# Performance work log

Hardware: AMD Instinct MI355X
Metric: run time of the kernel (lower is better)

Reference implementation:

```python
import math
import jax
import jax.numpy as jnp
import numpy as np

LMAX = 6                 # lmax
F8, F2 = 16, 64          # f_out//8, f_out//2 for f_out=128
DIM6 = sum((2 * l + 1) ** 2 for l in range(LMAX + 1))  # 455 = dim of so3_irreps(6)
NA = NB = NG = 16        # SO(3) activation grid (alpha, beta, gamma)
B, T, H, C = 32, 16, 4, 128


def _real_sh(lmax, xyz):
    # real spherical harmonics: (N,3) unit vectors -> (N,(lmax+1)^2), m=-l..l per l
    x, y, z = xyz[:, 0], xyz[:, 1], xyz[:, 2]
    st = np.sqrt(np.clip(1.0 - z * z, 0.0, None))
    phi = np.arctan2(y, x)
    n = xyz.shape[0]
    P = np.zeros((lmax + 1, lmax + 1, n))
    P[0, 0] = 1.0
    for m in range(1, lmax + 1):
        P[m, m] = -(2 * m - 1) * st * P[m - 1, m - 1]
    for m in range(lmax):
        P[m + 1, m] = (2 * m + 1) * z * P[m, m]
    for m in range(lmax + 1):
        for l in range(m + 2, lmax + 1):
            P[l, m] = ((2 * l - 1) * z * P[l - 1, m] - (l + m - 1) * P[l - 2, m]) / (l - m)
    cols = []
    for l in range(lmax + 1):
        for m in range(-l, l + 1):
            am = abs(m)
            K = math.sqrt((2 * l + 1) / (4 * math.pi) * math.factorial(l - am) / math.factorial(l + am))
            if m > 0:
                cols.append(math.sqrt(2.0) * K * np.cos(m * phi) * P[l, m])
            elif m < 0:
                cols.append(math.sqrt(2.0) * K * np.sin(am * phi) * P[l, am])
            else:
                cols.append(K * P[l, 0])
    return np.stack(cols, axis=-1)


def _flat_wigner(lmax, Rs):
    # component-normalized flat real Wigner-D basis: (G,3,3) -> (G, sum_l (2l+1)^2)
    # D_l(R) solved from Y_l(R x) = D_l(R) Y_l(x) by least squares in float64
    rng = np.random.default_rng(0)
    pts = rng.normal(size=(32, 3))
    pts /= np.linalg.norm(pts, axis=1, keepdims=True)
    Y = _real_sh(lmax, pts)                                     # (32,(lmax+1)^2)
    rp = np.einsum('gij,nj->gni', Rs, pts).reshape(-1, 3)
    Yr = _real_sh(lmax, rp).reshape(len(Rs), 32, -1)            # (G,32,(lmax+1)^2)
    blocks = []
    for l in range(lmax + 1):
        d = 2 * l + 1
        o = l * l
        Apinv = np.linalg.pinv(Y[:, o:o + d])                   # (d,32)
        D = np.einsum('kn,gnm->gmk', Apinv, Yr[:, :, o:o + d])  # (G,d,d)
        blocks.append(math.sqrt(d) * D.reshape(len(Rs), d * d))
    return np.concatenate(blocks, axis=-1)


def _rz(a):
    c, s = np.cos(a), np.sin(a)
    z, o = np.zeros_like(a), np.ones_like(a)
    return np.stack([np.stack([c, -s, z], -1), np.stack([s, c, z], -1), np.stack([z, z, o], -1)], -2)


def _ry(a):
    c, s = np.cos(a), np.sin(a)
    z, o = np.zeros_like(a), np.ones_like(a)
    return np.stack([np.stack([c, z, s], -1), np.stack([z, o, z], -1), np.stack([-s, z, c], -1)], -2)


def _so3_grid():
    # ZYZ Euler grid, Gauss-Legendre in beta; rotations (G,3,3) + Haar weights (G,) summing to 1
    nodes, wts = np.polynomial.legendre.leggauss(NB)
    betas = np.arccos(nodes)
    alphas = np.arange(NA) * 2 * np.pi / NA
    gammas = np.arange(NG) * 2 * np.pi / NG
    Aa, Bb, Cg = np.meshgrid(alphas, betas, gammas, indexing='ij')
    Rs = _rz(Aa.ravel()) @ _ry(Bb.ravel()) @ _rz(Cg.ravel())
    w = np.broadcast_to(wts[None, :, None], (NA, NB, NG)).ravel().copy()
    w *= (2 * np.pi / NA) * (2 * np.pi / NG) / (8 * np.pi ** 2)
    return Rs, w


def _ico_rotations():
    # the 60 rotations of the icosahedral group, generated by closure
    phi = (1.0 + 5.0 ** 0.5) / 2.0
    def rot(axis, ang):
        a = np.asarray(axis, dtype=np.float64)
        a = a / np.linalg.norm(a)
        K = np.array([[0.0, -a[2], a[1]], [a[2], 0.0, -a[0]], [-a[1], a[0], 0.0]])
        return np.eye(3) + math.sin(ang) * K + (1.0 - math.cos(ang)) * (K @ K)
    gens = [rot([0.0, 1.0, phi], 2.0 * np.pi / 5.0), rot([0.0, 0.0, 1.0], np.pi)]
    elems = [np.eye(3)]
    seen = {tuple(np.round(np.eye(3), 5).ravel())}
    frontier = list(elems)
    while frontier:
        nxt = []
        for R in frontier:
            for g in gens:
                Q = g @ R
                k = tuple(np.round(Q, 5).ravel())
                if k not in seen:
                    seen.add(k)
                    elems.append(Q)
                    nxt.append(Q)
        frontier = nxt
    return np.stack(elems)


def _equi_linear(xl, wl):
    # e3nn-style per-irrep linear: xl (...,f_in,u,m), wl (f_in,f_out,u,v); fan_in = f_in*u
    fan_in = wl.shape[0] * wl.shape[2]
    return jnp.einsum('...fum,fguv->...gvm', xl, wl) / np.sqrt(fan_in)


def _forward(x, trajectory, w1s, w1v, w2, D_in, D_outw, ico_wigners):
    b, t, _ = trajectory.shape
    # pack '1x0e+3x1e': scalar = traj[...,9], vectors = traj[...,:9]
    s = trajectory[..., 9][..., None, None, None]       # (b,t,f=1,u=1,m=1)
    v = trajectory[..., :9].reshape(b, t, 1, 3, 3)      # (b,t,f=1,u=3,m=3)
    h = jnp.concatenate([_equi_linear(s, w1s).reshape(b, t, F8, 1),
                         _equi_linear(v, w1v).reshape(b, t, F8, 9)], axis=-1)  # (b,t,16,10)
    # SO(3) activation: coeffs -> grid signal -> relu -> coeffs (lmax 1 -> 6)
    sig = jax.nn.relu(jnp.einsum('btci,gi->btcg', h, D_in))
    h = jnp.einsum('btcg,gi->btci', sig, D_outw)        # (b,t,16,455)
    # per-l equivariant linear, f 16 -> 64
    outs = []
    o = 0
    for l in range(LMAX + 1):
        d = 2 * l + 1
        xl = h[..., o:o + d * d].reshape(b, t, F8, d, d)
        outs.append(_equi_linear(xl, w2[l]).reshape(b, t, F2, d * d))
        o += d * d
    traj = jnp.concatenate(outs, axis=-1)               # (b,t,64,455)
    traj = jnp.einsum('bhcj,ij->bhci', traj, ico_wigners)  # sample on ico rotations
    xg = jnp.einsum('bhcj,ij->bhci', x, ico_wigners)
    return xg, traj


def setup_inputs():
    key = jax.random.key(0)
    ks = jax.random.split(key, 11)
    Rs, w = _so3_grid()
    D_in = _flat_wigner(1, Rs).astype(np.float32)                      # (G,10)
    D_outw = (_flat_wigner(LMAX, Rs) * w[:, None]).astype(np.float32)  # (G,455)
    ico = _flat_wigner(LMAX, _ico_rotations()).astype(np.float32)      # (60,455)
    inp = dict(
        x=jax.random.normal(ks[0], (B, H, C, DIM6), jnp.float32),
        trajectory=jax.random.normal(ks[1], (B, T, 10), jnp.float32),
        w1s=jax.random.normal(ks[2], (1, F8, 1, 1), jnp.float32),
        w1v=jax.random.normal(ks[3], (1, F8, 3, 3), jnp.float32),
        D_in=jnp.asarray(D_in),
        D_outw=jnp.asarray(D_outw),
        ico_wigners=jnp.asarray(ico),
    )
    for l in range(LMAX + 1):
        inp['w2_%d' % l] = jax.random.normal(ks[4 + l], (F8, F2, 2 * l + 1, 2 * l + 1), jnp.float32)
    return inp


def reference(x, trajectory, w1s, w1v, w2_0, w2_1, w2_2, w2_3, w2_4, w2_5, w2_6, D_in, D_outw, ico_wigners):
    w2 = [w2_0, w2_1, w2_2, w2_3, w2_4, w2_5, w2_6]
    return _forward(x, trajectory, w1s, w1v, w2, D_in, D_outw, ico_wigners)
```

## Files before the change

kernel.cpp:

```cpp
#include <hip/hip_runtime.h>
#include <math.h>


#define NBT  512
#define F8c  16
#define F2c  64
#define GJ   455
#define GG   4096
#define NICO 60
#define JP   512

typedef short bf16x8 __attribute__((ext_vector_type(8)));
typedef float f32x4  __attribute__((ext_vector_type(4)));
typedef unsigned int u32;
typedef unsigned short ushort;

struct W7 { const float* p[7]; };

__device__ __forceinline__ ushort f2bf(float f) {
  u32 u = __float_as_uint(f);
  return (ushort)((u + 0x7fffu + ((u >> 16) & 1u)) >> 16);
}

__device__ __forceinline__ int sel7(int l, int a0, int a1, int a2, int a3,
                                    int a4, int a5, int a6) {
  int r = a6;
  r = (l == 5) ? a5 : r; r = (l == 4) ? a4 : r; r = (l == 3) ? a3 : r;
  r = (l == 2) ? a2 : r; r = (l == 1) ? a1 : r; r = (l == 0) ? a0 : r;
  return r;
}
__device__ __forceinline__ float sel7f(int l, float a0, float a1, float a2,
                                       float a3, float a4, float a5, float a6) {
  float r = a6;
  r = (l == 5) ? a5 : r; r = (l == 4) ? a4 : r; r = (l == 3) ? a3 : r;
  r = (l == 2) ? a2 : r; r = (l == 1) ? a1 : r; r = (l == 0) ? a0 : r;
  return r;
}

__global__ __launch_bounds__(256) void k_pre(const float* __restrict__ traj,
                                             const float* __restrict__ w1s,
                                             const float* __restrict__ w1v,
                                             const float* __restrict__ ico,
                                             const float* __restrict__ Dout,
                                             W7 w2,
                                             float* __restrict__ h,
                                             ushort* __restrict__ icoB,
                                             ushort* __restrict__ icoBx,
                                             ushort* __restrict__ DoutBT,
                                             ushort* __restrict__ Abuf,
                                             ushort* __restrict__ Bbuf) {
  __shared__ float t[64][65];
  int b = blockIdx.x, tid = threadIdx.x;
  if (b < 2240) {
    ((uint4*)Abuf)[b * 256 + tid] = (uint4){0, 0, 0, 0};
  } else if (b < 2752) {
    int b2 = b - 2240;
    int jt = b2 & 7, kt = b2 >> 3;
    int tx = tid & 63, ty = tid >> 6;
    #pragma unroll
    for (int i = 0; i < 16; ++i) {
      int r = i * 4 + ty, j = jt * 64 + tx;
      t[r][tx] = (j < GJ) ? Dout[(size_t)(kt * 64 + r) * GJ + j] : 0.f;
    }
    __syncthreads();
    #pragma unroll
    for (int i = 0; i < 16; ++i) {
      int jl = i * 4 + ty;
      DoutBT[(size_t)(jt * 64 + jl) * GG + kt * 64 + tx] = f2bf(t[tx][jl]);
    }
  } else if (b < 4992) {
    int ee = (b - 2752) * 256 + tid;
    if (ee < 573440) {
      int l = (ee >= 4096) + (ee >= 16384) + (ee >= 57344) + (ee >= 114688) +
              (ee >= 225280) + (ee >= 360448);
      int base = sel7(l, 0, 4096, 16384, 57344, 114688, 225280, 360448);
      int d    = sel7(l, 1, 3, 5, 7, 9, 11, 13);
      int Kp   = sel7(l, 64, 64, 128, 128, 192, 192, 256);
      int local = ee - base;
      int row = local / Kp, kcol = local - row * Kp;
      int g2 = row / d, v = row - g2 * d;
      ushort val = 0;
      if (kcol < 16 * d) {
        int f = kcol / d, u = kcol - f * d;
        const float* wl = w2.p[l];
        float scl = rsqrtf(16.f * (float)d);
        val = f2bf(wl[(((size_t)f * 64 + g2) * d + u) * d + v] * scl);
      }
      Bbuf[ee] = val;
    }
  } else if (b < 5312) {
    int idx = (b - 4992) * 256 + tid;
    if (idx < NBT * 160) {
      int bt = idx / 160, r = idx % 160, c = r / 10, i = r % 10;
      const float* tr = traj + bt * 10;
      float val;
      if (i == 0) {
        val = tr[9] * w1s[c];
      } else {
        int k = i - 1, v = k / 3, m = k % 3;
        float s = 0.f;
        #pragma unroll
        for (int u = 0; u < 3; ++u) s = fmaf(tr[u * 3 + m], w1v[c * 9 + u * 3 + v], s);
        val = s * 0.57735026918962576f;
      }
      h[idx] = val;
    }
  } else if (b < 5440) {
    int e = (b - 5312) * 256 + tid;
    int i = e >> 9, k = e & 511;
    ushort val = 0;
    if (i < NICO && k < GJ) {
      int l = (k >= 1) + (k >= 10) + (k >= 35) + (k >= 84) + (k >= 165) + (k >= 286);
      int o = sel7(l, 0, 1, 10, 35, 84, 165, 286);
      int d = sel7(l, 1, 3, 5, 7, 9, 11, 13);
      float rcpd = sel7f(l, 1.f, 1.f / 3.f, 0.2f, 1.f / 7.f, 1.f / 9.f,
                         1.f / 11.f, 1.f / 13.f);
      int local = k - o;
      int m = (int)(((float)local + 0.5f) * rcpd);
      int v = local - m * d;
      val = f2bf(ico[i * GJ + o + v * d + m]);
    }
    icoB[e] = val;
  } else {
    int e = (b - 5440) * 256 + tid;
    int i = e >> 9, j = e & 511;
    icoBx[e] = (i < NICO && j < GJ) ? f2bf(ico[i * GJ + j]) : (ushort)0;
  }
}

__global__ __launch_bounds__(256) void k_sig(const float* __restrict__ h,
                                             const float* __restrict__ Din,
                                             ushort* __restrict__ sigb) {
  __shared__ float hs[160];
  int tid = threadIdx.x;
  int mb = blockIdx.y;
  int kt = blockIdx.x;
  if (tid < 160) hs[tid] = h[mb * 160 + tid];
  float dr[80];
  const float4* dp = (const float4*)(Din + (size_t)(kt * 2048 + tid * 8) * 10);
  #pragma unroll
  for (int q = 0; q < 20; ++q) {
    float4 v = dp[q];
    dr[q * 4 + 0] = v.x; dr[q * 4 + 1] = v.y; dr[q * 4 + 2] = v.z; dr[q * 4 + 3] = v.w;
  }
  __syncthreads();
  #pragma unroll
  for (int r = 0; r < 16; ++r) {
    float hv[10];
    #pragma unroll
    for (int i = 0; i < 10; ++i) hv[i] = hs[r * 10 + i];
    bf16x8 o;
    #pragma unroll
    for (int j = 0; j < 8; ++j) {
      float s = 0.f;
      #pragma unroll
      for (int i = 0; i < 10; ++i) s = fmaf(hv[i], dr[j * 10 + i], s);
      o[j] = (short)f2bf(fmaxf(s, 0.f));
    }
    *(bf16x8*)&sigb[((size_t)(mb * 16 + r)) * GG + kt * 2048 + tid * 8] = o;
  }
}

__global__ __launch_bounds__(256) void k_mm2s(const ushort* __restrict__ A,
                                              const ushort* __restrict__ Bm,
                                              float* __restrict__ part) {
  __shared__ __align__(16) short Asb[2][128 * 64];
  __shared__ __align__(16) short Bsb[2][128 * 64];
  int tid = threadIdx.x;
  int lane = tid & 63, wid = tid >> 6;
  int quad = lane >> 4, lr = lane & 15;
  int wm = wid >> 1, wn = wid & 1;
  int bid = blockIdx.x;
  int mb = bid & 63;
  int split = (bid >> 6) & 1;
  int nb = bid >> 7;
  int k0 = split * 2048;

  const ushort* Ab = A + (size_t)mb * 128 * GG + k0;
  const ushort* Bb = Bm + (size_t)nb * 128 * GG + k0;

  f32x4 acc[4][4];
  #pragma unroll
  for (int a = 0; a < 4; ++a)
    #pragma unroll
    for (int b = 0; b < 4; ++b) acc[a][b] = (f32x4){0.f, 0.f, 0.f, 0.f};

  auto stage = [&](int buf, int kc) {
    #pragma unroll
    for (int it = 0; it < 4; ++it) {
      int s0 = (wid * 4 + it) * 64;
      int s = s0 + lane;
      int r = s >> 3, pp = s & 7, p = pp ^ (r & 7);
      __builtin_amdgcn_global_load_lds(
          (const __attribute__((address_space(1))) u32*)(Ab + (size_t)r * GG + kc + p * 8),
          (__attribute__((address_space(3))) u32*)(&Asb[buf][s0 * 8]), 16, 0, 0);
    }
    #pragma unroll
    for (int it = 0; it < 4; ++it) {
      int s0 = (wid * 4 + it) * 64;
      int s = s0 + lane;
      int r = s >> 3, pp = s & 7, p = pp ^ (r & 7);
      __builtin_amdgcn_global_load_lds(
          (const __attribute__((address_space(1))) u32*)(Bb + (size_t)r * GG + kc + p * 8),
          (__attribute__((address_space(3))) u32*)(&Bsb[buf][s0 * 8]), 16, 0, 0);
    }
  };

  stage(0, 0);
  __syncthreads();
  for (int it = 0; it < 32; ++it) {
    int cur = it & 1;
    if (it < 31) stage(cur ^ 1, (it + 1) * 64);
    #pragma unroll
    for (int ks = 0; ks < 2; ++ks) {
      bf16x8 af[4], bv[4];
      #pragma unroll
      for (int mt = 0; mt < 4; ++mt) {
        int ra = wm * 64 + mt * 16 + lr;
        int v = (ks * 4 + quad) ^ (ra & 7);
        af[mt] = *(const bf16x8*)&Asb[cur][(ra * 8 + v) * 8];
      }
      #pragma unroll
      for (int nt = 0; nt < 4; ++nt) {
        int rb = wn * 64 + nt * 16 + lr;
        int v = (ks * 4 + quad) ^ (rb & 7);
        bv[nt] = *(const bf16x8*)&Bsb[cur][(rb * 8 + v) * 8];
      }
      #pragma unroll
      for (int mt = 0; mt < 4; ++mt)
        #pragma unroll
        for (int nt = 0; nt < 4; ++nt)
          acc[mt][nt] = __builtin_amdgcn_mfma_f32_16x16x32_bf16(af[mt], bv[nt], acc[mt][nt], 0, 0, 0);
    }
    __syncthreads();
  }
  #pragma unroll
  for (int mt = 0; mt < 4; ++mt)
    #pragma unroll
    for (int nt = 0; nt < 4; ++nt) {
      int j = nb * 128 + wn * 64 + nt * 16 + lr;
      #pragma unroll
      for (int r = 0; r < 4; ++r) {
        int m = mb * 128 + wm * 64 + mt * 16 + quad * 4 + r;
        part[((size_t)split * 8192 + m) * 512 + j] = acc[mt][nt][r];
      }
    }
}

__global__ __launch_bounds__(256) void k_red(const float* __restrict__ part,
                                             ushort* __restrict__ Abuf) {
  int t = blockIdx.x * 256 + threadIdx.x;
  int e0 = t * 8;
  int m = e0 >> 9, j0 = e0 & 511;
  const float4* p0 = (const float4*)(part + (size_t)m * 512 + j0);
  const float4* p1 = (const float4*)(part + (size_t)(8192 + m) * 512 + j0);
  float4 a0 = p0[0], a1 = p0[1], b0 = p1[0], b1 = p1[1];
  float s[8] = {a0.x + b0.x, a0.y + b0.y, a0.z + b0.z, a0.w + b0.w,
                a1.x + b1.x, a1.y + b1.y, a1.z + b1.z, a1.w + b1.w};
  int btg = m >> 4, f = m & 15;
  #pragma unroll
  for (int jj = 0; jj < 8; ++jj) {
    int j = j0 + jj;
    if (j < GJ) {
      int l = (j >= 1) + (j >= 10) + (j >= 35) + (j >= 84) + (j >= 165) + (j >= 286);
      int o    = sel7(l, 0, 1, 10, 35, 84, 165, 286);
      int d    = sel7(l, 1, 3, 5, 7, 9, 11, 13);
      int Kp   = sel7(l, 64, 64, 128, 128, 192, 192, 256);
      int Aoff = sel7(l, 0, 32768, 131072, 458752, 917504, 1802240, 2883584);
      float rcpd = sel7f(l, 1.f, 1.f / 3.f, 0.2f, 1.f / 7.f, 1.f / 9.f,
                         1.f / 11.f, 1.f / 13.f);
      int jl = j - o;
      int u = (int)(((float)jl + 0.5f) * rcpd);
      int mB = jl - u * d;
      Abuf[(size_t)Aoff + ((size_t)btg * d + mB) * Kp + f * d + u] = f2bf(s[jj]);
    }
  }
}

__global__ __launch_bounds__(256) void k_mm2f(const ushort* __restrict__ A,
                                              const ushort* __restrict__ Bm,
                                              ushort* __restrict__ Abuf) {
  __shared__ __align__(16) short Asb[2][128 * 64];
  __shared__ __align__(16) short Bsb[2][128 * 64];
  int tid = threadIdx.x;
  int lane = tid & 63, wid = tid >> 6;
  int quad = lane >> 4, lr = lane & 15;
  int wm = wid >> 1, wn = wid & 1;
  int bid = blockIdx.x;
  int mb = bid & 63, nb = bid >> 6;
  f32x4 acc[4][4];
  #pragma unroll
  for (int a = 0; a < 4; ++a)
    #pragma unroll
    for (int b = 0; b < 4; ++b) acc[a][b] = (f32x4){0.f, 0.f, 0.f, 0.f};
  const ushort* Ab = A + (size_t)mb * 128 * GG;
  const ushort* Bb = Bm + (size_t)nb * 128 * GG;
  auto stage = [&](int buf, int kc) {
    #pragma unroll
    for (int it = 0; it < 4; ++it) {
      int s0 = (wid * 4 + it) * 64;
      int s = s0 + lane;
      int r = s >> 3, pp = s & 7, p = pp ^ (r & 7);
      __builtin_amdgcn_global_load_lds(
          (const __attribute__((address_space(1))) u32*)(Ab + (size_t)r * GG + kc + p * 8),
          (__attribute__((address_space(3))) u32*)(&Asb[buf][s0 * 8]), 16, 0, 0);
    }
    #pragma unroll
    for (int it = 0; it < 4; ++it) {
      int s0 = (wid * 4 + it) * 64;
      int s = s0 + lane;
      int r = s >> 3, pp = s & 7, p = pp ^ (r & 7);
      __builtin_amdgcn_global_load_lds(
          (const __attribute__((address_space(1))) u32*)(Bb + (size_t)r * GG + kc + p * 8),
          (__attribute__((address_space(3))) u32*)(&Bsb[buf][s0 * 8]), 16, 0, 0);
    }
  };
  stage(0, 0);
  __syncthreads();
  for (int it = 0; it < 64; ++it) {
    int cur = it & 1;
    if (it < 63) stage(cur ^ 1, (it + 1) * 64);
    #pragma unroll
    for (int ks = 0; ks < 2; ++ks) {
      bf16x8 af[4], bvv[4];
      #pragma unroll
      for (int mt = 0; mt < 4; ++mt) {
        int ra = wm * 64 + mt * 16 + lr;
        int v = (ks * 4 + quad) ^ (ra & 7);
        af[mt] = *(const bf16x8*)&Asb[cur][(ra * 8 + v) * 8];
      }
      #pragma unroll
      for (int nt = 0; nt < 4; ++nt) {
        int rb = wn * 64 + nt * 16 + lr;
        int v = (ks * 4 + quad) ^ (rb & 7);
        bvv[nt] = *(const bf16x8*)&Bsb[cur][(rb * 8 + v) * 8];
      }
      #pragma unroll
      for (int mt = 0; mt < 4; ++mt)
        #pragma unroll
        for (int nt = 0; nt < 4; ++nt)
          acc[mt][nt] = __builtin_amdgcn_mfma_f32_16x16x32_bf16(af[mt], bvv[nt], acc[mt][nt], 0, 0, 0);
    }
    __syncthreads();
  }
  #pragma unroll
  for (int nt = 0; nt < 4; ++nt) {
    int j = nb * 128 + wn * 64 + nt * 16 + lr;
    if (j < GJ) {
      int l = (j >= 1) + (j >= 10) + (j >= 35) + (j >= 84) + (j >= 165) + (j >= 286);
      int o    = sel7(l, 0, 1, 10, 35, 84, 165, 286);
      int d    = sel7(l, 1, 3, 5, 7, 9, 11, 13);
      int Kp   = sel7(l, 64, 64, 128, 128, 192, 192, 256);
      int Aoff = sel7(l, 0, 32768, 131072, 458752, 917504, 1802240, 2883584);
      int jl = j - o;
      float rcpd = 1.0f / (float)d;
      int u = (int)(((float)jl + 0.5f) * rcpd);
      int mB = jl - u * d;
      #pragma unroll
      for (int mt = 0; mt < 4; ++mt)
        #pragma unroll
        for (int r = 0; r < 4; ++r) {
          int m = mb * 128 + wm * 64 + mt * 16 + quad * 4 + r;
          int btg = m >> 4, f = m & 15;
          Abuf[(size_t)Aoff + ((size_t)btg * d + mB) * Kp + f * d + u] =
              f2bf(acc[mt][nt][r]);
        }
    }
  }
}

__global__ __launch_bounds__(256) void k_batchX(const ushort* __restrict__ Abuf,
                                                const ushort* __restrict__ Bbuf,
                                                const float* __restrict__ x,
                                                const ushort* __restrict__ icoBx,
                                                ushort* __restrict__ trajbf,
                                                float* __restrict__ xg) {
  __shared__ __align__(16) short As[2][128 * 64];
  __shared__ __align__(16) short Bs[2][128 * 64];
  int bid = blockIdx.x;
  int tid = threadIdx.x;
  int lane = tid & 63, wid = tid >> 6;
  int quad = lane >> 4, lr = lane & 15;
  int wm = wid >> 1, wn = wid & 1;
  f32x4 acc[4][4];
  #pragma unroll
  for (int a = 0; a < 4; ++a)
    #pragma unroll
    for (int b = 0; b < 4; ++b) acc[a][b] = (f32x4){0.f, 0.f, 0.f, 0.f};

  if (bid >= 1008) {
    int mtile = bid - 1008;
    auto loadx = [&](int itk, float* xv) {
      #pragma unroll
      for (int g = 0; g < 4; ++g) {
        int s = g * 256 + tid;
        int r = s >> 3, p8 = s & 7, p = p8 ^ (r & 7);
        const float* xr = x + (size_t)(mtile * 128 + r) * GJ;
        int j0 = itk * 64 + p * 8;
        #pragma unroll
        for (int jj = 0; jj < 8; ++jj) {
          int j = j0 + jj;
          xv[g * 8 + jj] = (j < GJ) ? xr[j] : 0.f;
        }
      }
    };
    auto writex = [&](int buf, const float* xv) {
      #pragma unroll
      for (int g = 0; g < 4; ++g) {
        int s = g * 256 + tid;
        bf16x8 v8;
        #pragma unroll
        for (int jj = 0; jj < 8; ++jj) v8[jj] = (short)f2bf(xv[g * 8 + jj]);
        *(bf16x8*)&As[buf][s * 8] = v8;
      }
    };
    auto stageBx = [&](int buf, int kc) {
      #pragma unroll
      for (int it = 0; it < 2; ++it) {
        int s0 = (wid * 2 + it) * 64;
        int s = s0 + lane;
        int r = s >> 3, p8 = s & 7, p = p8 ^ (r & 7);
        const ushort* gb = icoBx + (size_t)r * JP + kc + p * 8;
        __builtin_amdgcn_global_load_lds(
            (const __attribute__((address_space(1))) u32*)gb,
            (__attribute__((address_space(3))) u32*)(&Bs[buf][s0 * 8]), 16, 0, 0);
      }
    };
    float xv[32];
    loadx(0, xv);
    writex(0, xv);
    stageBx(0, 0);
    __syncthreads();
    for (int it = 0; it < 8; ++it) {
      int cur = it & 1;
      float xn[32];
      if (it < 7) {
        loadx(it + 1, xn);
        stageBx(cur ^ 1, (it + 1) * 64);
      }
      #pragma unroll
      for (int ks = 0; ks < 2; ++ks) {
        bf16x8 af[4], bv[2];
        #pragma unroll
        for (int mt = 0; mt < 4; ++mt) {
          int ra = wm * 64 + mt * 16 + lr;
          int v = (ks * 4 + quad) ^ (ra & 7);
          af[mt] = *(const bf16x8*)&As[cur][(ra * 8 + v) * 8];
        }
        #pragma unroll
        for (int nt = 0; nt < 2; ++nt) {
          int rb = wn * 32 + nt * 16 + lr;
          int v = (ks * 4 + quad) ^ (rb & 7);
          bv[nt] = *(const bf16x8*)&Bs[cur][(rb * 8 + v) * 8];
        }
        #pragma unroll
        for (int mt = 0; mt < 4; ++mt)
          #pragma unroll
          for (int nt = 0; nt < 2; ++nt)
            acc[mt][nt] = __builtin_amdgcn_mfma_f32_16x16x32_bf16(af[mt], bv[nt], acc[mt][nt], 0, 0, 0);
      }
      if (it < 7) writex(cur ^ 1, xn);
      __syncthreads();
    }
    #pragma unroll
    for (int mt = 0; mt < 4; ++mt)
      #pragma unroll
      for (int nt = 0; nt < 2; ++nt) {
        int i = wn * 32 + nt * 16 + lr;
        if (i < NICO) {
          #pragma unroll
          for (int r = 0; r < 4; ++r) {
            int row = mtile * 128 + wm * 64 + mt * 16 + quad * 4 + r;
            xg[(size_t)row * NICO + i] = acc[mt][nt][r];
          }
        }
      }
    return;
  }

  int l = (bid >= 4) + (bid >= 28) + (bid >= 88) + (bid >= 200) +
          (bid >= 380) + (bid >= 644);
  int bbase = sel7(l, 0, 4, 28, 88, 200, 380, 644);
  int d     = sel7(l, 1, 3, 5, 7, 9, 11, 13);
  int Kp    = sel7(l, 64, 64, 128, 128, 192, 192, 256);
  int o     = sel7(l, 0, 1, 10, 35, 84, 165, 286);
  int Aoff  = sel7(l, 0, 32768, 131072, 458752, 917504, 1802240, 2883584);
  int Boff  = sel7(l, 0, 4096, 16384, 57344, 114688, 225280, 360448);
  int ntc   = sel7(l, 1, 2, 3, 4, 5, 6, 7);
  float rcpntc = sel7f(l, 1.f, 0.5f, 1.f / 3.f, 0.25f, 0.2f, 1.f / 6.f, 1.f / 7.f);
  float rcpd   = sel7f(l, 1.f, 1.f / 3.f, 0.2f, 1.f / 7.f, 1.f / 9.f,
                       1.f / 11.f, 1.f / 13.f);
  int t = bid - bbase;
  int mtile = (int)(((float)t + 0.5f) * rcpntc);
  int ntile = t - mtile * ntc;
  int Nl = 64 * d;

  const ushort* Ab = Abuf + Aoff + (size_t)mtile * 128 * Kp;
  const ushort* Bb = Bbuf + Boff + (size_t)ntile * 128 * Kp;

  auto stage = [&](int buf, int kc) {
    #pragma unroll
    for (int it = 0; it < 4; ++it) {
      int s0 = (wid * 4 + it) * 64;
      int s = s0 + lane;
      int r = s >> 3, pp = s & 7, p = pp ^ (r & 7);
      __builtin_amdgcn_global_load_lds(
          (const __attribute__((address_space(1))) u32*)(Ab + (size_t)r * Kp + kc + p * 8),
          (__attribute__((address_space(3))) u32*)(&As[buf][s0 * 8]), 16, 0, 0);
    }
    #pragma unroll
    for (int it = 0; it < 4; ++it) {
      int s0 = (wid * 4 + it) * 64;
      int s = s0 + lane;
      int r = s >> 3, pp = s & 7, p = pp ^ (r & 7);
      __builtin_amdgcn_global_load_lds(
          (const __attribute__((address_space(1))) u32*)(Bb + (size_t)r * Kp + kc + p * 8),
          (__attribute__((address_space(3))) u32*)(&Bs[buf][s0 * 8]), 16, 0, 0);
    }
  };

  int nIter = Kp >> 6;
  stage(0, 0);
  __syncthreads();
  for (int it = 0; it < nIter; ++it) {
    int cur = it & 1;
    if (it + 1 < nIter) stage(cur ^ 1, (it + 1) * 64);
    #pragma unroll
    for (int ks = 0; ks < 2; ++ks) {
      bf16x8 af[4], bv[4];
      #pragma unroll
      for (int mt = 0; mt < 4; ++mt) {
        int ra = wm * 64 + mt * 16 + lr;
        int v = (ks * 4 + quad) ^ (ra & 7);
        af[mt] = *(const bf16x8*)&As[cur][(ra * 8 + v) * 8];
      }
      #pragma unroll
      for (int nt = 0; nt < 4; ++nt) {
        int rb = wn * 64 + nt * 16 + lr;
        int v = (ks * 4 + quad) ^ (rb & 7);
        bv[nt] = *(const bf16x8*)&Bs[cur][(rb * 8 + v) * 8];
      }
      #pragma unroll
      for (int mt = 0; mt < 4; ++mt)
        #pragma unroll
        for (int nt = 0; nt < 4; ++nt)
          acc[mt][nt] = __builtin_amdgcn_mfma_f32_16x16x32_bf16(af[mt], bv[nt], acc[mt][nt], 0, 0, 0);
    }
    __syncthreads();
  }
  #pragma unroll
  for (int nt = 0; nt < 4; ++nt) {
    int Ncol = ntile * 128 + wn * 64 + nt * 16 + lr;
    if (Ncol < Nl) {
      int g2 = (int)(((float)Ncol + 0.5f) * rcpd);
      int v = Ncol - g2 * d;
      #pragma unroll
      for (int mt = 0; mt < 4; ++mt)
        #pragma unroll
        for (int r = 0; r < 4; ++r) {
          int Mrow = mtile * 128 + wm * 64 + mt * 16 + quad * 4 + r;
          int bt = (int)(((float)Mrow + 0.5f) * rcpd);
          int m = Mrow - bt * d;
          trajbf[(size_t)(bt * 64 + g2) * JP + o + m * d + v] = f2bf(acc[mt][nt][r]);
        }
    }
  }
}

__global__ __launch_bounds__(256) void k_icoT(const ushort* __restrict__ trajbf,
                                              const ushort* __restrict__ icoB,
                                              float* __restrict__ trajo) {
  __shared__ __align__(16) short As[2][128 * 64];
  __shared__ __align__(16) short Bs[2][64 * 64];
  int mtile = blockIdx.x;
  int tid = threadIdx.x;
  int lane = tid & 63, wid = tid >> 6;
  int quad = lane >> 4, lr = lane & 15;
  int wm = wid >> 1, wn = wid & 1;
  f32x4 acc[4][2];
  #pragma unroll
  for (int a = 0; a < 4; ++a)
    #pragma unroll
    for (int b = 0; b < 2; ++b) acc[a][b] = (f32x4){0.f, 0.f, 0.f, 0.f};

  auto stage = [&](int buf, int kc) {
    #pragma unroll
    for (int it = 0; it < 4; ++it) {
      int s0 = (wid * 4 + it) * 64;
      int s = s0 + lane;
      int r = s >> 3, p8 = s & 7, p = p8 ^ (r & 7);
      const ushort* ga = trajbf + (size_t)(mtile * 128 + r) * JP + kc + p * 8;
      __builtin_amdgcn_global_load_lds(
          (const __attribute__((address_space(1))) u32*)ga,
          (__attribute__((address_space(3))) u32*)(&As[buf][s0 * 8]), 16, 0, 0);
    }
    #pragma unroll
    for (int it = 0; it < 2; ++it) {
      int s0 = (wid * 2 + it) * 64;
      int s = s0 + lane;
      int r = s >> 3, p8 = s & 7, p = p8 ^ (r & 7);
      const ushort* gb = icoB + (size_t)r * JP + kc + p * 8;
      __builtin_amdgcn_global_load_lds(
          (const __attribute__((address_space(1))) u32*)gb,
          (__attribute__((address_space(3))) u32*)(&Bs[buf][s0 * 8]), 16, 0, 0);
    }
  };

  stage(0, 0);
  __syncthreads();
  for (int it = 0; it < 8; ++it) {
    int cur = it & 1;
    if (it < 7) stage(cur ^ 1, (it + 1) * 64);
    #pragma unroll
    for (int ks = 0; ks < 2; ++ks) {
      bf16x8 af[4], bv[2];
      #pragma unroll
      for (int mt = 0; mt < 4; ++mt) {
        int ra = wm * 64 + mt * 16 + lr;
        int v = (ks * 4 + quad) ^ (ra & 7);
        af[mt] = *(const bf16x8*)&As[cur][(ra * 8 + v) * 8];
      }
      #pragma unroll
      for (int nt = 0; nt < 2; ++nt) {
        int rb = wn * 32 + nt * 16 + lr;
        int v = (ks * 4 + quad) ^ (rb & 7);
        bv[nt] = *(const bf16x8*)&Bs[cur][(rb * 8 + v) * 8];
      }
      #pragma unroll
      for (int mt = 0; mt < 4; ++mt)
        #pragma unroll
        for (int nt = 0; nt < 2; ++nt)
          acc[mt][nt] = __builtin_amdgcn_mfma_f32_16x16x32_bf16(af[mt], bv[nt], acc[mt][nt], 0, 0, 0);
    }
    __syncthreads();
  }
  #pragma unroll
  for (int mt = 0; mt < 4; ++mt)
    #pragma unroll
    for (int nt = 0; nt < 2; ++nt) {
      int i = wn * 32 + nt * 16 + lr;
      if (i < NICO) {
        #pragma unroll
        for (int r = 0; r < 4; ++r) {
          int row = mtile * 128 + wm * 64 + mt * 16 + quad * 4 + r;
          trajo[(size_t)row * NICO + i] = acc[mt][nt][r];
        }
      }
    }
}

extern "C" void kernel_launch(void* const* d_in, const int* in_sizes, int n_in,
                              void* d_out, int out_size, void* d_ws, size_t ws_size,
                              hipStream_t stream) {
  const float *x = nullptr, *traj = nullptr, *w1s = nullptr, *w1v = nullptr;
  const float *Din = nullptr, *Dout = nullptr, *ico = nullptr;
  W7 w2{};
  for (int i = 0; i < n_in; ++i) {
    const float* p = (const float*)d_in[i];
    switch (in_sizes[i]) {
      case 7454720: x = p; break;
      case 5120:    traj = p; break;
      case 16:      w1s = p; break;
      case 144:     w1v = p; break;
      case 40960:   Din = p; break;
      case 1863680: Dout = p; break;
      case 27300:   ico = p; break;
      case 1024:    w2.p[0] = p; break;
      case 9216:    w2.p[1] = p; break;
      case 25600:   w2.p[2] = p; break;
      case 50176:   w2.p[3] = p; break;
      case 82944:   w2.p[4] = p; break;
      case 123904:  w2.p[5] = p; break;
      case 173056:  w2.p[6] = p; break;
      default: break;
    }
  }
  char* wsb = (char*)d_ws;
  float*  h       = (float*)wsb;
  ushort* DoutBT  = (ushort*)(wsb + 327680);
  ushort* icoB    = (ushort*)(wsb + 4521984);
  ushort* icoBx   = (ushort*)(wsb + 4587520);
  ushort* Abuf    = (ushort*)(wsb + 4653056);
  ushort* Bbuf    = (ushort*)(wsb + 13828096);
  ushort* sigb    = (ushort*)(wsb + 14974976);
  ushort* trajbf  = sigb;
  float*  part    = (float*)(wsb + 82083840);
  float* xg    = (float*)d_out;
  float* trajo = (float*)d_out + 983040;

  k_pre<<<dim3(5568), dim3(256), 0, stream>>>(traj, w1s, w1v, ico, Dout, w2,
                                              h, icoB, icoBx, DoutBT, Abuf, Bbuf);
  k_sig<<<dim3(2, 512), dim3(256), 0, stream>>>(h, Din, sigb);
  if (ws_size >= 115638272ULL) {
    k_mm2s<<<dim3(512),  dim3(256), 0, stream>>>(sigb, DoutBT, part);
    k_red <<<dim3(2048), dim3(256), 0, stream>>>(part, Abuf);
  } else {
    k_mm2f<<<dim3(256),  dim3(256), 0, stream>>>(sigb, DoutBT, Abuf);
  }
  k_batchX<<<dim3(1136), dim3(256), 0, stream>>>(Abuf, Bbuf, x, icoBx, trajbf, xg);
  k_icoT  <<<dim3(256),  dim3(256), 0, stream>>>(trajbf, icoB, trajo);
}
```

Baseline: 236.0 us.

## Single-buffer LDS in GEMM kernels and store split-K partials as bf16

Drops LDS double buffering in k_batchX and k_icoT so they load, sync, then compute. This halves shared memory per block to allow more resident blocks. It also narrows acc to [4][2] in the ico branch, which cuts register use. Split-K partials in k_mm2s/k_red are now stored as bf16 instead of fp32, halving that intermediate traffic. The trade-offs are lost load/compute overlap within a block and an extra rounding step before the partial sums are added.

```diff
diff --git a/kernel.cpp b/kernel.cpp
--- a/kernel.cpp
+++ b/kernel.cpp
@@ -20,6 +20,9 @@
 __device__ __forceinline__ ushort f2bf(float f) {
   u32 u = __float_as_uint(f);
   return (ushort)((u + 0x7fffu + ((u >> 16) & 1u)) >> 16);
+}
+__device__ __forceinline__ float bf2f(ushort v) {
+  return __uint_as_float(((u32)v) << 16);
 }
 
 __device__ __forceinline__ int sel7(int l, int a0, int a1, int a2, int a3,
@@ -163,7 +166,7 @@
 
 __global__ __launch_bounds__(256) void k_mm2s(const ushort* __restrict__ A,
                                               const ushort* __restrict__ Bm,
-                                              float* __restrict__ part) {
+                                              ushort* __restrict__ part) {
   __shared__ __align__(16) short Asb[2][128 * 64];
   __shared__ __align__(16) short Bsb[2][128 * 64];
   int tid = threadIdx.x;
@@ -242,21 +245,22 @@
       #pragma unroll
       for (int r = 0; r < 4; ++r) {
         int m = mb * 128 + wm * 64 + mt * 16 + quad * 4 + r;
-        part[((size_t)split * 8192 + m) * 512 + j] = acc[mt][nt][r];
-      }
-    }
-}
-
-__global__ __launch_bounds__(256) void k_red(const float* __restrict__ part,
+        part[((size_t)split * 8192 + m) * 512 + j] = f2bf(acc[mt][nt][r]);
+      }
+    }
+}
+
+__global__ __launch_bounds__(256) void k_red(const ushort* __restrict__ part,
                                              ushort* __restrict__ Abuf) {
   int t = blockIdx.x * 256 + threadIdx.x;
   int e0 = t * 8;
   int m = e0 >> 9, j0 = e0 & 511;
-  const float4* p0 = (const float4*)(part + (size_t)m * 512 + j0);
-  const float4* p1 = (const float4*)(part + (size_t)(8192 + m) * 512 + j0);
-  float4 a0 = p0[0], a1 = p0[1], b0 = p1[0], b1 = p1[1];
-  float s[8] = {a0.x + b0.x, a0.y + b0.y, a0.z + b0.z, a0.w + b0.w,
-                a1.x + b1.x, a1.y + b1.y, a1.z + b1.z, a1.w + b1.w};
+  bf16x8 a0 = *(const bf16x8*)(part + (size_t)m * 512 + j0);
+  bf16x8 b0 = *(const bf16x8*)(part + (size_t)(8192 + m) * 512 + j0);
+  float s[8];
+  #pragma unroll
+  for (int i = 0; i < 8; ++i)
+    s[i] = bf2f((ushort)a0[i]) + bf2f((ushort)b0[i]);
   int btg = m >> 4, f = m & 15;
   #pragma unroll
   for (int jj = 0; jj < 8; ++jj) {
@@ -375,22 +379,23 @@
                                                 const ushort* __restrict__ icoBx,
                                                 ushort* __restrict__ trajbf,
                                                 float* __restrict__ xg) {
-  __shared__ __align__(16) short As[2][128 * 64];
-  __shared__ __align__(16) short Bs[2][128 * 64];
+  __shared__ __align__(16) short As[128 * 64];
+  __shared__ __align__(16) short Bs[128 * 64];
   int bid = blockIdx.x;
   int tid = threadIdx.x;
   int lane = tid & 63, wid = tid >> 6;
   int quad = lane >> 4, lr = lane & 15;
   int wm = wid >> 1, wn = wid & 1;
-  f32x4 acc[4][4];
-  #pragma unroll
-  for (int a = 0; a < 4; ++a)
-    #pragma unroll
-    for (int b = 0; b < 4; ++b) acc[a][b] = (f32x4){0.f, 0.f, 0.f, 0.f};
 
   if (bid >= 1008) {
     int mtile = bid - 1008;
-    auto loadx = [&](int itk, float* xv) {
+    f32x4 acc[4][2];
+    #pragma unroll
+    for (int a = 0; a < 4; ++a)
+      #pragma unroll
+      for (int b = 0; b < 2; ++b) acc[a][b] = (f32x4){0.f, 0.f, 0.f, 0.f};
+    float xn[32];
+    auto loadx = [&](int itk) {
       #pragma unroll
       for (int g = 0; g < 4; ++g) {
         int s = g * 256 + tid;
@@ -400,21 +405,21 @@
         #pragma unroll
         for (int jj = 0; jj < 8; ++jj) {
           int j = j0 + jj;
-          xv[g * 8 + jj] = (j < GJ) ? xr[j] : 0.f;
+          xn[g * 8 + jj] = (j < GJ) ? xr[j] : 0.f;
         }
       }
     };
-    auto writex = [&](int buf, const float* xv) {
+    auto writex = [&]() {
       #pragma unroll
       for (int g = 0; g < 4; ++g) {
         int s = g * 256 + tid;
         bf16x8 v8;
         #pragma unroll
-        for (int jj = 0; jj < 8; ++jj) v8[jj] = (short)f2bf(xv[g * 8 + jj]);
-        *(bf16x8*)&As[buf][s * 8] = v8;
+        for (int jj = 0; jj < 8; ++jj) v8[jj] = (short)f2bf(xn[g * 8 + jj]);
+        *(bf16x8*)&As[s * 8] = v8;
       }
     };
-    auto stageBx = [&](int buf, int kc) {
+    auto stageBx = [&](int kc) {
       #pragma unroll
       for (int it = 0; it < 2; ++it) {
         int s0 = (wid * 2 + it) * 64;
@@ -423,21 +428,13 @@
         const ushort* gb = icoBx + (size_t)r * JP + kc + p * 8;
         __builtin_amdgcn_global_load_lds(
             (const __attribute__((address_space(1))) u32*)gb,
-            (__attribute__((address_space(3))) u32*)(&Bs[buf][s0 * 8]), 16, 0, 0);
+            (__attribute__((address_space(3))) u32*)(Bs + s0 * 8), 16, 0, 0);
       }
     };
-    float xv[32];
-    loadx(0, xv);
-    writex(0, xv);
-    stageBx(0, 0);
+    loadx(0); writex(); stageBx(0);
     __syncthreads();
     for (int it = 0; it < 8; ++it) {
-      int cur = it & 1;
-      float xn[32];
-      if (it < 7) {
-        loadx(it + 1, xn);
-        stageBx(cur ^ 1, (it + 1) * 64);
-      }
+      if (it < 7) loadx(it + 1);
       #pragma unroll
       for (int ks = 0; ks < 2; ++ks) {
         bf16x8 af[4], bv[2];
@@ -445,13 +442,13 @@
         for (int mt = 0; mt < 4; ++mt) {
           int ra = wm * 64 + mt * 16 + lr;
           int v = (ks * 4 + quad) ^ (ra & 7);
-          af[mt] = *(const bf16x8*)&As[cur][(ra * 8 + v) * 8];
+          af[mt] = *(const bf16x8*)&As[(ra * 8 + v) * 8];
         }
         #pragma unroll
         for (int nt = 0; nt < 2; ++nt) {
           int rb = wn * 32 + nt * 16 + lr;
           int v = (ks * 4 + quad) ^ (rb & 7);
-          bv[nt] = *(const bf16x8*)&Bs[cur][(rb * 8 + v) * 8];
+          bv[nt] = *(const bf16x8*)&Bs[(rb * 8 + v) * 8];
         }
         #pragma unroll
         for (int mt = 0; mt < 4; ++mt)
@@ -459,8 +456,12 @@
           for (int nt = 0; nt < 2; ++nt)
             acc[mt][nt] = __builtin_amdgcn_mfma_f32_16x16x32_bf16(af[mt], bv[nt], acc[mt][nt], 0, 0, 0);
       }
-      if (it < 7) writex(cur ^ 1, xn);
-      __syncthreads();
+      if (it < 7) {
+        __syncthreads();
+        writex();
+        stageBx((it + 1) * 64);
+        __syncthreads();
+      }
     }
     #pragma unroll
     for (int mt = 0; mt < 4; ++mt)
@@ -477,6 +478,12 @@
       }
     return;
   }
+
+  f32x4 acc[4][4];
+  #pragma unroll
+  for (int a = 0; a < 4; ++a)
+    #pragma unroll
+    for (int b = 0; b < 4; ++b) acc[a][b] = (f32x4){0.f, 0.f, 0.f, 0.f};
 
   int l = (bid >= 4) + (bid >= 28) + (bid >= 88) + (bid >= 200) +
           (bid >= 380) + (bid >= 644);
@@ -498,7 +505,7 @@
   const ushort* Ab = Abuf + Aoff + (size_t)mtile * 128 * Kp;
   const ushort* Bb = Bbuf + Boff + (size_t)ntile * 128 * Kp;
 
-  auto stage = [&](int buf, int kc) {
+  auto stage = [&](int kc) {
     #pragma unroll
     for (int it = 0; it < 4; ++it) {
       int s0 = (wid * 4 + it) * 64;
@@ -506,7 +513,7 @@
       int r = s >> 3, pp = s & 7, p = pp ^ (r & 7);
       __builtin_amdgcn_global_load_lds(
           (const __attribute__((address_space(1))) u32*)(Ab + (size_t)r * Kp + kc + p * 8),
-          (__attribute__((address_space(3))) u32*)(&As[buf][s0 * 8]), 16, 0, 0);
+          (__attribute__((address_space(3))) u32*)(As + s0 * 8), 16, 0, 0);
     }
     #pragma unroll
     for (int it = 0; it < 4; ++it) {
@@ -515,16 +522,15 @@
       int r = s >> 3, pp = s & 7, p = pp ^ (r & 7);
       __builtin_amdgcn_global_load_lds(
           (const __attribute__((address_space(1))) u32*)(Bb + (size_t)r * Kp + kc + p * 8),
-          (__attribute__((address_space(3))) u32*)(&Bs[buf][s0 * 8]), 16, 0, 0);
+          (__attribute__((address_space(3))) u32*)(Bs + s0 * 8), 16, 0, 0);
     }
   };
 
   int nIter = Kp >> 6;
-  stage(0, 0);
-  __syncthreads();
   for (int it = 0; it < nIter; ++it) {
-    int cur = it & 1;
-    if (it + 1 < nIter) stage(cur ^ 1, (it + 1) * 64);
+    if (it) __syncthreads();
+    stage(it * 64);
+    __syncthreads();
     #pragma unroll
     for (int ks = 0; ks < 2; ++ks) {
       bf16x8 af[4], bv[4];
@@ -532,13 +538,13 @@
       for (int mt = 0; mt < 4; ++mt) {
         int ra = wm * 64 + mt * 16 + lr;
         int v = (ks * 4 + quad) ^ (ra & 7);
-        af[mt] = *(const bf16x8*)&As[cur][(ra * 8 + v) * 8];
+        af[mt] = *(const bf16x8*)&As[(ra * 8 + v) * 8];
       }
       #pragma unroll
       for (int nt = 0; nt < 4; ++nt) {
         int rb = wn * 64 + nt * 16 + lr;
         int v = (ks * 4 + quad) ^ (rb & 7);
-        bv[nt] = *(const bf16x8*)&Bs[cur][(rb * 8 + v) * 8];
+        bv[nt] = *(const bf16x8*)&Bs[(rb * 8 + v) * 8];
       }
       #pragma unroll
       for (int mt = 0; mt < 4; ++mt)
@@ -546,7 +552,6 @@
         for (int nt = 0; nt < 4; ++nt)
           acc[mt][nt] = __builtin_amdgcn_mfma_f32_16x16x32_bf16(af[mt], bv[nt], acc[mt][nt], 0, 0, 0);
     }
-    __syncthreads();
   }
   #pragma unroll
   for (int nt = 0; nt < 4; ++nt) {
@@ -570,8 +575,8 @@
 __global__ __launch_bounds__(256) void k_icoT(const ushort* __restrict__ trajbf,
                                               const ushort* __restrict__ icoB,
                                               float* __restrict__ trajo) {
-  __shared__ __align__(16) short As[2][128 * 64];
-  __shared__ __align__(16) short Bs[2][64 * 64];
+  __shared__ __align__(16) short As[128 * 64];
+  __shared__ __align__(16) short Bs[64 * 64];
   int mtile = blockIdx.x;
   int tid = threadIdx.x;
   int lane = tid & 63, wid = tid >> 6;
@@ -583,7 +588,7 @@
     #pragma unroll
     for (int b = 0; b < 2; ++b) acc[a][b] = (f32x4){0.f, 0.f, 0.f, 0.f};
 
-  auto stage = [&](int buf, int kc) {
+  auto stage = [&](int kc) {
     #pragma unroll
     for (int it = 0; it < 4; ++it) {
       int s0 = (wid * 4 + it) * 64;
@@ -592,7 +597,7 @@
       const ushort* ga = trajbf + (size_t)(mtile * 128 + r) * JP + kc + p * 8;
       __builtin_amdgcn_global_load_lds(
           (const __attribute__((address_space(1))) u32*)ga,
-          (__attribute__((address_space(3))) u32*)(&As[buf][s0 * 8]), 16, 0, 0);
+          (__attribute__((address_space(3))) u32*)(As + s0 * 8), 16, 0, 0);
     }
     #pragma unroll
     for (int it = 0; it < 2; ++it) {
@@ -602,15 +607,14 @@
       const ushort* gb = icoB + (size_t)r * JP + kc + p * 8;
       __builtin_amdgcn_global_load_lds(
           (const __attribute__((address_space(1))) u32*)gb,
-          (__attribute__((address_space(3))) u32*)(&Bs[buf][s0 * 8]), 16, 0, 0);
+          (__attribute__((address_space(3))) u32*)(Bs + s0 * 8), 16, 0, 0);
     }
   };
 
-  stage(0, 0);
-  __syncthreads();
   for (int it = 0; it < 8; ++it) {
-    int cur = it & 1;
-    if (it < 7) stage(cur ^ 1, (it + 1) * 64);
+    if (it) __syncthreads();
+    stage(it * 64);
+    __syncthreads();
     #pragma unroll
     for (int ks = 0; ks < 2; ++ks) {
       bf16x8 af[4], bv[2];
@@ -618,13 +622,13 @@
       for (int mt = 0; mt < 4; ++mt) {
         int ra = wm * 64 + mt * 16 + lr;
         int v = (ks * 4 + quad) ^ (ra & 7);
-        af[mt] = *(const bf16x8*)&As[cur][(ra * 8 + v) * 8];
+        af[mt] = *(const bf16x8*)&As[(ra * 8 + v) * 8];
       }
       #pragma unroll
       for (int nt = 0; nt < 2; ++nt) {
         int rb = wn * 32 + nt * 16 + lr;
         int v = (ks * 4 + quad) ^ (rb & 7);
-        bv[nt] = *(const bf16x8*)&Bs[cur][(rb * 8 + v) * 8];
+        bv[nt] = *(const bf16x8*)&Bs[(rb * 8 + v) * 8];
       }
       #pragma unroll
       for (int mt = 0; mt < 4; ++mt)
@@ -632,7 +636,6 @@
         for (int nt = 0; nt < 2; ++nt)
           acc[mt][nt] = __builtin_amdgcn_mfma_f32_16x16x32_bf16(af[mt], bv[nt], acc[mt][nt], 0, 0, 0);
     }
-    __syncthreads();
   }
   #pragma unroll
   for (int mt = 0; mt < 4; ++mt)
@@ -684,7 +687,7 @@
   ushort* Bbuf    = (ushort*)(wsb + 13828096);
   ushort* sigb    = (ushort*)(wsb + 14974976);
   ushort* trajbf  = sigb;
-  float*  part    = (float*)(wsb + 82083840);
+  ushort* part    = (ushort*)(wsb + 82083840);
   float* xg    = (float*)d_out;
   float* trajo = (float*)d_out + 983040;
 
```

After: 236.8 us. No clear change (+0.4%).
